# Kernel optimization log

Hardware: AMD Instinct MI355X
Metric: run time of the kernel (lower is better)

Reference implementation:

```python
import jax, jax.numpy as jnp
import numpy as np

N_NODES = 8192
K = 32

def setup_inputs() -> dict:
    key = jax.random.key(0)
    kA, kI = jax.random.split(key)
    A = jax.random.normal(kA, (N_NODES, N_NODES), dtype=jnp.float32)
    idx = jnp.arange(N_NODES, dtype=jnp.int64)  # unused by forward, kept for signature fidelity
    return {"A": A, "idx": idx}

def reference(A, idx):
    # adj = relu(A)
    adj = jax.nn.relu(A)
    # row-wise top-k indices, scatter 1.0 into a zero mask, multiply
    _, indices = jax.lax.top_k(adj, K)            # [N, K]
    rows = jnp.arange(adj.shape[0])[:, None]      # [N, 1]
    mask = jnp.zeros_like(adj).at[rows, indices].set(1.0)
    return adj * mask
```

## Files before the change

kernel.cpp:

```cpp
#include <hip/hip_runtime.h>


constexpr int N     = 8192;
constexpr int K     = 32;
constexpr int NBINS = 2048;
constexpr int CAP   = 256;
constexpr int BLOCK = 256;
constexpr int SLOTS = CAP / 64;
constexpr float TSPEC     = 2.0f;
constexpr int   SPEC_BASE = 1024;

typedef float f4 __attribute__((ext_vector_type(4)));

template<int PER>
__device__ __forceinline__ bool find_cutoff(const unsigned* hist, int lane,
                                            int base, int& B, int& G) {
    unsigned s = 0;
    #pragma unroll
    for (int i = 0; i < PER; ++i)
        s += hist[base + lane * PER + ((i + lane) & (PER - 1))];
    unsigned acc = s;
    #pragma unroll
    for (int off = 1; off < 64; off <<= 1) {
        unsigned t = __shfl_down(acc, off, 64);
        if (lane + off < 64) acc += t;
    }
    unsigned long long m = __ballot(acc >= (unsigned)K);
    if (m == 0ull) return false;
    int g = 63 - __clzll((long long)m);
    unsigned above = (g < 63) ? (unsigned)__shfl((int)acc, g + 1, 64) : 0u;
    unsigned h  = (lane < PER) ? hist[base + g * PER + lane] : 0u;
    unsigned a2 = h;
    #pragma unroll
    for (int off = 1; off < 64; off <<= 1) {
        unsigned t = __shfl_down(a2, off, 64);
        if (lane + off < 64) a2 += t;
    }
    unsigned long long m2 = __ballot(above + a2 >= (unsigned)K);
    int bl = 63 - __clzll((long long)m2);
    B = base + g * PER + bl;
    G = (int)(above + (unsigned)__shfl((int)a2, bl, 64)
                    - (unsigned)__shfl((int)h,  bl, 64));
    return true;
}

__global__ __launch_bounds__(BLOCK)
void topk_relu_kernel(const float* __restrict__ A, float* __restrict__ Out) {
    const int row  = blockIdx.x;
    const int tid  = threadIdx.x;
    const int lane = tid & 63;

    __shared__ unsigned hist[NBINS];
    __shared__ float    cand_val[CAP];
    __shared__ int      cand_col[CAP];
    __shared__ unsigned cand_cnt;

    #pragma unroll
    for (int i = 0; i < (NBINS - SPEC_BASE) / BLOCK; ++i)
        hist[SPEC_BASE + tid + i * BLOCK] = 0u;
    if (tid == 0) cand_cnt = 0u;
    __syncthreads();

    const f4* __restrict__ Arow = reinterpret_cast<const f4*>(A + (size_t)row * N);
    f4 vf[8];
    #pragma unroll
    for (int i = 0; i < 8; ++i) vf[i] = Arow[i * BLOCK + tid];

    #pragma unroll
    for (int i = 0; i < 8; ++i) {
        #pragma unroll
        for (int c = 0; c < 4; ++c) {
            float f = vf[i][c];
            if (f > TSPEC) atomicAdd(&hist[__float_as_uint(f) >> 20], 1u);
        }
    }
    __syncthreads();

    int B, G;
    bool ok = find_cutoff<16>(hist, lane, SPEC_BASE, B, G);
    if (!ok) {
        __syncthreads();
        #pragma unroll
        for (int i = 0; i < NBINS / BLOCK; ++i) hist[tid + i * BLOCK] = 0u;
        __syncthreads();
        #pragma unroll
        for (int i = 0; i < 8; ++i) {
            #pragma unroll
            for (int c = 0; c < 4; ++c) {
                float f = vf[i][c];
                if (f > 0.0f) atomicAdd(&hist[__float_as_uint(f) >> 20], 1u);
            }
        }
        __syncthreads();
        if (!find_cutoff<32>(hist, lane, 0, B, G)) { B = -1; G = 0; }
    }
    const int R = K - G;

    if (B >= 0) {
        #pragma unroll
        for (int i = 0; i < 8; ++i) {
            #pragma unroll
            for (int c = 0; c < 4; ++c) {
                float f = vf[i][c];
                if (f > 0.0f && (int)(__float_as_uint(f) >> 20) == B) {
                    unsigned ix = atomicAdd(&cand_cnt, 1u);
                    if (ix < CAP) {
                        cand_val[ix] = f;
                        cand_col[ix] = (i * BLOCK + tid) * 4 + c;
                    }
                }
            }
        }
    }
    __syncthreads();

    float vR = 0.0f;
    int   cR = -1;
    if (B >= 0) {
        vR = __int_as_float(0x7f800000);
        const int C = (int)min(cand_cnt, (unsigned)CAP);
        float mv[SLOTS]; int mc[SLOTS]; int rk[SLOTS];
        #pragma unroll
        for (int s = 0; s < SLOTS; ++s) {
            const int j = lane + s * 64;
            if (j < C) { mv[s] = cand_val[j]; mc[s] = cand_col[j]; }
            else       { mv[s] = -1.0f;       mc[s] = 0x7fffffff; }
            rk[s] = 0;
        }
        for (int j = 0; j < C; ++j) {
            const float vj = cand_val[j];
            const int   cj = cand_col[j];
            #pragma unroll
            for (int s = 0; s < SLOTS; ++s)
                if (vj > mv[s] || (vj == mv[s] && cj < mc[s])) rk[s]++;
        }
        float bv = 0.0f; int bc = -1; bool found = false;
        #pragma unroll
        for (int s = 0; s < SLOTS; ++s)
            if (lane + s * 64 < C && rk[s] == R - 1) { bv = mv[s]; bc = mc[s]; found = true; }
        unsigned long long bm = __ballot(found);
        if (bm != 0ull) {
            int src = (int)__ffsll((long long)bm) - 1;
            vR = __shfl(bv, src, 64);
            cR = __shfl(bc, src, 64);
        }
    }

    float* __restrict__ Orow = Out + (size_t)row * N;
    #pragma unroll
    for (int i = 0; i < 8; ++i) {
        f4 w;
        #pragma unroll
        for (int c = 0; c < 4; ++c) {
            float f   = vf[i][c];
            int   col = (i * BLOCK + tid) * 4 + c;
            bool keep = (f > vR) || (f == vR && col <= cR);
            w[c] = keep ? f : 0.0f;
        }
        __builtin_nontemporal_store(w, reinterpret_cast<f4*>(Orow) + i * BLOCK + tid);
    }
}

extern "C" void kernel_launch(void* const* d_in, const int* in_sizes, int n_in,
                              void* d_out, int out_size, void* d_ws, size_t ws_size,
                              hipStream_t stream) {
    const float* A   = (const float*)d_in[0];
    float*       Out = (float*)d_out;
    (void)in_sizes; (void)n_in; (void)d_ws; (void)ws_size; (void)out_size;
    topk_relu_kernel<<<dim3(N), dim3(BLOCK), 0, stream>>>(A, Out);
}
```

Measured before the change: 92.24 us.

## Collect speculative candidates during histogram pass and compact cutoff bin before ranking

Candidates above the speculative threshold are now captured during the first histogram pass, which removes the separate scan of the row to gather cutoff-bin values. The cutoff-bin entries are then compacted with a ballot into a small buffer (up to 128) so the rank loop runs over fewer elements with two slots per lane. The row is no longer held in registers; it is re-read from global memory (hopefully served from cache) in the fallback and output passes. This trades register pressure for extra loads and adds an atomic per candidate in the main pass.

New measurement: 108.6 us. +17.7%, slower.

```diff
diff --git a/kernel.cpp b/kernel.cpp
--- a/kernel.cpp
+++ b/kernel.cpp
@@ -4,11 +4,12 @@
 constexpr int N     = 8192;
 constexpr int K     = 32;
 constexpr int NBINS = 2048;
-constexpr int CAP   = 256;
+constexpr int SPEC_BASE = 1024;
+constexpr int CAP   = 512;
+constexpr int SLOTS = CAP / 64;
+constexpr int BB    = 128;
 constexpr int BLOCK = 256;
-constexpr int SLOTS = CAP / 64;
-constexpr float TSPEC     = 2.0f;
-constexpr int   SPEC_BASE = 1024;
+constexpr float TSPEC = 2.0f;
 
 typedef float f4 __attribute__((ext_vector_type(4)));
 
@@ -51,93 +52,108 @@
     const int lane = tid & 63;
 
     __shared__ unsigned hist[NBINS];
-    __shared__ float    cand_val[CAP];
-    __shared__ int      cand_col[CAP];
-    __shared__ unsigned cand_cnt;
+    __shared__ float    cv[CAP];
+    __shared__ int      cc[CAP];
+    __shared__ float    bbv[BB];
+    __shared__ int      bbc[BB];
+    __shared__ unsigned ccnt;
 
     #pragma unroll
     for (int i = 0; i < (NBINS - SPEC_BASE) / BLOCK; ++i)
         hist[SPEC_BASE + tid + i * BLOCK] = 0u;
-    if (tid == 0) cand_cnt = 0u;
+    if (tid == 0) ccnt = 0u;
     __syncthreads();
 
     const f4* __restrict__ Arow = reinterpret_cast<const f4*>(A + (size_t)row * N);
-    f4 vf[8];
-    #pragma unroll
-    for (int i = 0; i < 8; ++i) vf[i] = Arow[i * BLOCK + tid];
-
     #pragma unroll
     for (int i = 0; i < 8; ++i) {
+        f4 v = Arow[i * BLOCK + tid];
         #pragma unroll
         for (int c = 0; c < 4; ++c) {
-            float f = vf[i][c];
-            if (f > TSPEC) atomicAdd(&hist[__float_as_uint(f) >> 20], 1u);
+            float f = v[c];
+            if (f > TSPEC) {
+                atomicAdd(&hist[__float_as_uint(f) >> 20], 1u);
+                unsigned ix = atomicAdd(&ccnt, 1u);
+                if (ix < CAP) { cv[ix] = f; cc[ix] = (i * BLOCK + tid) * 4 + c; }
+            }
         }
     }
     __syncthreads();
 
     int B, G;
     bool ok = find_cutoff<16>(hist, lane, SPEC_BASE, B, G);
-    if (!ok) {
+    unsigned Call = ccnt;
+    if (!ok || Call > (unsigned)CAP) {
         __syncthreads();
         #pragma unroll
         for (int i = 0; i < NBINS / BLOCK; ++i) hist[tid + i * BLOCK] = 0u;
+        if (tid == 0) ccnt = 0u;
         __syncthreads();
         #pragma unroll
         for (int i = 0; i < 8; ++i) {
+            f4 v = Arow[i * BLOCK + tid];
             #pragma unroll
             for (int c = 0; c < 4; ++c) {
-                float f = vf[i][c];
+                float f = v[c];
                 if (f > 0.0f) atomicAdd(&hist[__float_as_uint(f) >> 20], 1u);
             }
         }
         __syncthreads();
         if (!find_cutoff<32>(hist, lane, 0, B, G)) { B = -1; G = 0; }
-    }
-    const int R = K - G;
-
-    if (B >= 0) {
-        #pragma unroll
-        for (int i = 0; i < 8; ++i) {
+        if (B >= 0) {
             #pragma unroll
-            for (int c = 0; c < 4; ++c) {
-                float f = vf[i][c];
-                if (f > 0.0f && (int)(__float_as_uint(f) >> 20) == B) {
-                    unsigned ix = atomicAdd(&cand_cnt, 1u);
-                    if (ix < CAP) {
-                        cand_val[ix] = f;
-                        cand_col[ix] = (i * BLOCK + tid) * 4 + c;
+            for (int i = 0; i < 8; ++i) {
+                f4 v = Arow[i * BLOCK + tid];
+                #pragma unroll
+                for (int c = 0; c < 4; ++c) {
+                    float f = v[c];
+                    if (f > 0.0f && (int)(__float_as_uint(f) >> 20) == B) {
+                        unsigned ix = atomicAdd(&ccnt, 1u);
+                        if (ix < CAP) { cv[ix] = f; cc[ix] = (i * BLOCK + tid) * 4 + c; }
                     }
                 }
             }
         }
+        __syncthreads();
+        Call = ccnt;
     }
-    __syncthreads();
+    const int R = K - G;
 
     float vR = 0.0f;
     int   cR = -1;
     if (B >= 0) {
-        vR = __int_as_float(0x7f800000);
-        const int C = (int)min(cand_cnt, (unsigned)CAP);
-        float mv[SLOTS]; int mc[SLOTS]; int rk[SLOTS];
+        const int C = (int)min(Call, (unsigned)CAP);
+        int total = 0;
         #pragma unroll
         for (int s = 0; s < SLOTS; ++s) {
             const int j = lane + s * 64;
-            if (j < C) { mv[s] = cand_val[j]; mc[s] = cand_col[j]; }
-            else       { mv[s] = -1.0f;       mc[s] = 0x7fffffff; }
-            rk[s] = 0;
+            bool flag = false; float fv = 0.0f; int fc = 0;
+            if (j < C) {
+                fv = cv[j];
+                if ((int)(__float_as_uint(fv) >> 20) == B) { flag = true; fc = cc[j]; }
+            }
+            unsigned long long m = __ballot(flag);
+            if (flag) {
+                int pos = total + __popcll(m & ((1ull << lane) - 1ull));
+                if (pos < BB) { bbv[pos] = fv; bbc[pos] = fc; }
+            }
+            total += (int)__popcll(m);
         }
-        for (int j = 0; j < C; ++j) {
-            const float vj = cand_val[j];
-            const int   cj = cand_col[j];
-            #pragma unroll
-            for (int s = 0; s < SLOTS; ++s)
-                if (vj > mv[s] || (vj == mv[s] && cj < mc[s])) rk[s]++;
+        const int T = min(total, BB);
+        float mv0 = -1.0f, mv1 = -1.0f; int mc0 = 0x7fffffff, mc1 = 0x7fffffff;
+        if (lane      < T) { mv0 = bbv[lane];      mc0 = bbc[lane]; }
+        if (lane + 64 < T) { mv1 = bbv[lane + 64]; mc1 = bbc[lane + 64]; }
+        int r0 = 0, r1 = 0;
+        for (int j = 0; j < T; ++j) {
+            const float vj = bbv[j];
+            const int   cj = bbc[j];
+            if (vj > mv0 || (vj == mv0 && cj < mc0)) r0++;
+            if (vj > mv1 || (vj == mv1 && cj < mc1)) r1++;
         }
         float bv = 0.0f; int bc = -1; bool found = false;
-        #pragma unroll
-        for (int s = 0; s < SLOTS; ++s)
-            if (lane + s * 64 < C && rk[s] == R - 1) { bv = mv[s]; bc = mc[s]; found = true; }
+        if (lane      < T && r0 == R - 1) { bv = mv0; bc = mc0; found = true; }
+        if (lane + 64 < T && r1 == R - 1) { bv = mv1; bc = mc1; found = true; }
+        vR = __int_as_float(0x7f800000);
         unsigned long long bm = __ballot(found);
         if (bm != 0ull) {
             int src = (int)__ffsll((long long)bm) - 1;
@@ -149,13 +165,13 @@
     float* __restrict__ Orow = Out + (size_t)row * N;
     #pragma unroll
     for (int i = 0; i < 8; ++i) {
+        f4 v = Arow[i * BLOCK + tid];
         f4 w;
         #pragma unroll
         for (int c = 0; c < 4; ++c) {
-            float f   = vf[i][c];
+            float f   = v[c];
             int   col = (i * BLOCK + tid) * 4 + c;
-            bool keep = (f > vR) || (f == vR && col <= cR);
-            w[c] = keep ? f : 0.0f;
+            w[c] = ((f > vR) || (f == vR && col <= cR)) ? f : 0.0f;
         }
         __builtin_nontemporal_store(w, reinterpret_cast<f4*>(Orow) + i * BLOCK + tid);
     }
```
